# Kernel tuning notes

Measured on AMD Instinct MI355X. Metric: run time of the kernel, lower is better.

The kernel has to match this reference:

```python
import itertools, math
import jax, jax.numpy as jnp
import numpy as np

N_QUBITS = 8
N_LAYERS = 2
D = 2 ** N_QUBITS
B = 16384
PAIRS = list(itertools.combinations(range(N_QUBITS), 2))
N_PAIRS = len(PAIRS)


def _static():
    s = np.arange(D)
    # ising_masks[p, s] = +1 if bits qi,qj of s differ else -1
    masks = np.stack([
        np.where((((s >> (N_QUBITS - 1 - qi)) & 1) ^ ((s >> (N_QUBITS - 1 - qj)) & 1)).astype(bool), 1.0, -1.0).astype(np.float32)
        for qi, qj in PAIRS])
    # z_signs[k, s] = +1 if bit k of s is 0 else -1
    zsig = np.stack([
        np.where(((s >> (N_QUBITS - 1 - k)) & 1).astype(bool), -1.0, 1.0).astype(np.float32)
        for k in range(N_QUBITS)])
    # CNOT is a permutation: src[i] = i ^ target_mask if ctrl bit of i set, else i
    cidx = np.empty((N_LAYERS, N_QUBITS, D), np.int32)
    for l in range(N_LAYERS):
        rng = l % (N_QUBITS - 1) + 1 if N_QUBITS > 1 else 1
        for ctrl in range(N_QUBITS):
            tgt = (ctrl + rng) % N_QUBITS
            bit = ((s >> (N_QUBITS - 1 - ctrl)) & 1).astype(bool)
            cidx[l, ctrl] = np.where(bit, s ^ (1 << (N_QUBITS - 1 - tgt)), s)
    return jnp.asarray(masks), jnp.asarray(zsig), jnp.asarray(cidx)

ISING_MASKS, Z_SIGNS, CNOT_IDX = _static()


def _ry(a):
    # a: [...] -> [..., 2, 2] complex64
    c, sn = jnp.cos(a * 0.5), jnp.sin(a * 0.5)
    return jnp.stack([jnp.stack([c, -sn], -1), jnp.stack([sn, c], -1)], -2).astype(jnp.complex64)


def _rz(a):
    h = a.astype(jnp.complex64) * 0.5
    z = jnp.zeros_like(h)
    return jnp.stack([jnp.stack([jnp.exp(-1j * h), z], -1), jnp.stack([z, jnp.exp(1j * h)], -1)], -2)


def _rot(w):
    # w: [3] = (phi, theta, omega) -> Rot = RZ(omega) @ RY(theta) @ RZ(phi), shape [2,2]
    return _rz(w[2]) @ _ry(w[1]) @ _rz(w[0])


def _apply_1q(state, gate, k):
    # state: [B, D]; gate: [B,2,2] (batched) or [2,2] (shared)
    Bs, Ds = state.shape
    hi, lo = 1 << k, 1 << (N_QUBITS - k - 1)
    s = state.reshape(Bs, hi, 2, lo)
    if gate.ndim == 3:
        s = jnp.einsum('bij,bhjl->bhil', gate, s)
    else:
        s = jnp.einsum('ij,bhjl->bhil', gate, s)
    return s.reshape(Bs, Ds)


def _forward(theta, phi_enc, j_upper, vqc_weights):
    Bs = theta.shape[0]
    state = jnp.zeros((Bs, D), jnp.complex64).at[:, 0].set(1.0)
    # encoding layer
    for k in range(N_QUBITS):
        state = _apply_1q(state, _ry(theta[:, k]), k)
        state = _apply_1q(state, _rz(phi_enc[:, k]), k)
    # IsingZZ: product over pairs of exp(0.5j*pi*J_p*mask_p) == exp of sum
    exponent = (0.5 * math.pi) * (j_upper @ ISING_MASKS)  # [B, D], real
    state = state * jnp.exp(1j * exponent.astype(jnp.complex64))
    for l in range(N_LAYERS):
        for k in range(N_QUBITS):
            state = _apply_1q(state, _rot(vqc_weights[l, k]), k)
        for k in range(N_QUBITS):
            # CNOT ring as gather permutation (same math as state @ cnot.mT)
            state = jnp.take(state, CNOT_IDX[l, k], axis=1)
        if l < N_LAYERS - 1:
            for k in range(N_QUBITS):
                state = _apply_1q(state, _ry(theta[:, k] * 0.5), k)
                state = _apply_1q(state, _rz(phi_enc[:, k] * 0.5), k)
    probs = jnp.abs(state) ** 2  # [B, D] float32
    return (probs @ Z_SIGNS.T).astype(theta.dtype)  # [B, N_QUBITS]


def setup_inputs() -> dict:
    key = jax.random.key(0)
    k1, k2, k3, k4 = jax.random.split(key, 4)
    return {
        'theta': jax.random.normal(k1, (B, N_QUBITS), jnp.float32),
        'phi_enc': jax.random.normal(k2, (B, N_QUBITS), jnp.float32),
        'j_upper': jax.random.normal(k3, (B, N_PAIRS), jnp.float32),
        'vqc_weights': jax.random.normal(k4, (N_LAYERS, N_QUBITS, 3), jnp.float32),
    }


def reference(theta, phi_enc, j_upper, vqc_weights):
    return _forward(theta, phi_enc, j_upper, vqc_weights)
```

## Files before the change

### kernel.cpp

```cpp
#include <hip/hip_runtime.h>


using f2 = __attribute__((ext_vector_type(2))) float;

__device__ __forceinline__ f2 pkfma(f2 a, f2 b, f2 c) {
#if __has_builtin(__builtin_elementwise_fma)
    return __builtin_elementwise_fma(a, b, c);
#else
    f2 r; r.x = fmaf(a.x, b.x, c.x); r.y = fmaf(a.y, b.y, c.y); return r;
#endif
}

__device__ __forceinline__ f2 cmul2(f2 w, f2 z) {
    const f2 wr = (f2){w.x, w.x};
    const f2 wi = (f2){-w.y, w.y};
    const f2 zs = (f2){z.y, z.x};
    return pkfma(wi, zs, wr * z);
}
__device__ __forceinline__ f2 cmadd(f2 acc, f2 w, f2 z) {
    const f2 wr = (f2){w.x, w.x};
    const f2 wi = (f2){-w.y, w.y};
    const f2 zs = (f2){z.y, z.x};
    return pkfma(wi, zs, pkfma(wr, z, acc));
}

__device__ __forceinline__ f2 shflx(f2 v, int m) {
    f2 r; r.x = __shfl_xor(v.x, m, 64); r.y = __shfl_xor(v.y, m, 64); return r;
}

__device__ __forceinline__ f2 enc_sel(float t, float p, bool hi) {
    float s_, c_, sp_, cp_;
    __sincosf(t * 0.5f, &s_, &c_);
    __sincosf(p * 0.5f, &sp_, &cp_);
    const float m = hi ? s_ : c_;
    f2 r; r.x = m * cp_; r.y = hi ? m * sp_ : -m * sp_;
    return r;
}

template<int VREG, int VLANE, int UREG, int ULANE>
__device__ __forceinline__ void gate16(f2 (&s)[16], int lane16,
                                       f2 g00, f2 g01, f2 g10, f2 g11)
{
    f2 a0, b0, a1, b1;
    if constexpr (ULANE != 0) {
        const bool lp = (__popc(lane16 & ULANE) & 1) != 0;
        a0 = lp ? g11 : g00;  b0 = lp ? g10 : g01;
        a1 = lp ? g00 : g11;  b1 = lp ? g01 : g10;
    } else {
        a0 = g00; b0 = g01; a1 = g11; b1 = g10;
    }
    constexpr bool flip = (__builtin_popcount(VREG & UREG) & 1) != 0;
    if constexpr (VLANE == 0) {
        constexpr int pivot = VREG & (-VREG);
        #pragma unroll
        for (int j = 0; j < 16; ++j) {
            if ((j & pivot) != 0) continue;
            const int j2 = j ^ VREG;
            const bool cJ = (__builtin_popcount(j & UREG) & 1) != 0;
            const bool cK = cJ ^ flip;
            const f2 x = s[j], y = s[j2];
            const f2 A = cJ ? a1 : a0, B = cJ ? b1 : b0;
            const f2 C = cK ? a1 : a0, D = cK ? b1 : b0;
            s[j]  = cmadd(cmul2(A, x), B, y);
            s[j2] = cmadd(cmul2(C, y), D, x);
        }
    } else if constexpr (VREG == 0) {
        #pragma unroll
        for (int j = 0; j < 16; ++j) {
            const f2 p = shflx(s[j], VLANE);
            const bool cJ = (__builtin_popcount(j & UREG) & 1) != 0;
            const f2 A = cJ ? a1 : a0, B = cJ ? b1 : b0;
            s[j] = cmadd(cmul2(A, s[j]), B, p);
        }
    } else {
        constexpr int pivot = VREG & (-VREG);
        #pragma unroll
        for (int j = 0; j < 16; ++j) {
            if ((j & pivot) != 0) continue;
            const int j2 = j ^ VREG;
            const f2 p1 = shflx(s[j2], VLANE);
            const f2 p2 = shflx(s[j],  VLANE);
            const bool cJ = (__builtin_popcount(j & UREG) & 1) != 0;
            const bool cK = cJ ^ flip;
            const f2 A = cJ ? a1 : a0, B = cJ ? b1 : b0;
            const f2 C = cK ? a1 : a0, D = cK ? b1 : b0;
            s[j]  = cmadd(cmul2(A, s[j]),  B, p1);
            s[j2] = cmadd(cmul2(C, s[j2]), D, p2);
        }
    }
}

#define ROT0(K, VR, VL, UR, UL) do {                                    \
    const float* g_ = gates + (K)*8;                                    \
    const f2 R00={g_[0],g_[1]}, R01={g_[2],g_[3]};                      \
    const f2 R10={g_[4],g_[5]}, R11={g_[6],g_[7]};                      \
    gate16<VR, VL, UR, UL>(s, lane16, R00, R01, R10, R11);              \
} while (0)

#define FUSED(K, VR, VL, UR, UL) do {                                   \
    const float* g_ = gates + (8 + (K))*8;                              \
    const f2 R00={g_[0],g_[1]}, R01={g_[2],g_[3]};                      \
    const f2 R10={g_[4],g_[5]}, R11={g_[6],g_[7]};                      \
    float c_, s_, cp_, sp_;                                             \
    __sincosf(th[K] * 0.25f, &s_, &c_);                                 \
    __sincosf(ph[K] * 0.25f, &sp_, &cp_);                               \
    const f2 E00={ c_*cp_, -c_*sp_}, E01={-s_*cp_,  s_*sp_};            \
    const f2 E10={ s_*cp_,  s_*sp_}, E11={ c_*cp_,  c_*sp_};            \
    const f2 F00 = cmadd(cmul2(R00, E00), R01, E10);                    \
    const f2 F01 = cmadd(cmul2(R00, E01), R01, E11);                    \
    const f2 F10 = cmadd(cmul2(R10, E00), R11, E10);                    \
    const f2 F11 = cmadd(cmul2(R10, E01), R11, E11);                    \
    gate16<VR, VL, UR, UL>(s, lane16, F00, F01, F10, F11);              \
} while (0)

__global__ __launch_bounds__(64) void prep_gates(const float* __restrict__ w,
                                                 float* __restrict__ g)
{
    const int t = threadIdx.x;
    if (t < 16) {
        const float wph = w[t*3+0], wth = w[t*3+1], wom = w[t*3+2];
        float c_, s_, ca_, sa_, cb_, sb_;
        __sincosf(wth * 0.5f, &s_, &c_);
        __sincosf(0.5f * (wph + wom), &sa_, &ca_);
        __sincosf(0.5f * (wph - wom), &sb_, &cb_);
        float* o = g + t * 8;
        o[0] =  c_*ca_;  o[1] = -c_*sa_;
        o[2] = -s_*cb_;  o[3] = -s_*sb_;
        o[4] =  s_*cb_;  o[5] = -s_*sb_;
        o[6] =  c_*ca_;  o[7] =  c_*sa_;
    }
}

__global__ __launch_bounds__(64, 4) void vqc_kernel(
    const float* __restrict__ theta,
    const float* __restrict__ phi,
    const float* __restrict__ jup,
    const float* __restrict__ gates,
    float* __restrict__ out,
    int Btot)
{
    const int wid    = blockIdx.x;
    const int lane   = threadIdx.x & 63;
    const int lane16 = lane & 15;
    const int bq     = wid * 4 + (lane >> 4);
    const int b      = bq < Btot ? bq : Btot - 1;

    float th[8], ph[8];
    {
        const float4* t4 = reinterpret_cast<const float4*>(theta + (size_t)b * 8);
        const float4* p4 = reinterpret_cast<const float4*>(phi   + (size_t)b * 8);
        const float4 a = t4[0], c = t4[1], d = p4[0], e = p4[1];
        th[0]=a.x; th[1]=a.y; th[2]=a.z; th[3]=a.w;
        th[4]=c.x; th[5]=c.y; th[6]=c.z; th[7]=c.w;
        ph[0]=d.x; ph[1]=d.y; ph[2]=d.z; ph[3]=d.w;
        ph[4]=e.x; ph[5]=e.y; ph[6]=e.z; ph[7]=e.w;
    }

    f2 P = enc_sel(th[4], ph[4], (lane16 & 8) != 0);
    P = cmul2(P, enc_sel(th[5], ph[5], (lane16 & 4) != 0));
    P = cmul2(P, enc_sel(th[6], ph[6], (lane16 & 2) != 0));
    P = cmul2(P, enc_sel(th[7], ph[7], (lane16 & 1) != 0));

    f2 m01[4], m23[4];
    {
        float s0, c0, sp0, cp0, s1, c1, sp1, cp1;
        __sincosf(th[0]*0.5f, &s0, &c0); __sincosf(ph[0]*0.5f, &sp0, &cp0);
        __sincosf(th[1]*0.5f, &s1, &c1); __sincosf(ph[1]*0.5f, &sp1, &cp1);
        const f2 A0={c0*cp0,-c0*sp0}, A1={s0*cp0,s0*sp0};
        const f2 B0={c1*cp1,-c1*sp1}, B1={s1*cp1,s1*sp1};
        #pragma unroll
        for (int a = 0; a < 4; ++a)
            m01[a] = cmul2((a & 2) ? A1 : A0, (a & 1) ? B1 : B0);
        __sincosf(th[2]*0.5f, &s0, &c0); __sincosf(ph[2]*0.5f, &sp0, &cp0);
        __sincosf(th[3]*0.5f, &s1, &c1); __sincosf(ph[3]*0.5f, &sp1, &cp1);
        const f2 C0={c0*cp0,-c0*sp0}, C1={s0*cp0,s0*sp0};
        const f2 D0={c1*cp1,-c1*sp1}, D1={s1*cp1,s1*sp1};
        #pragma unroll
        for (int a = 0; a < 4; ++a)
            m23[a] = cmul2((a & 2) ? C1 : C0, (a & 1) ? D1 : D0);
    }

    float c01, c02, c03, c12, c13, c23, Q0, Q1, Q2, Q3, LL;
    {
        const float4* J4 = reinterpret_cast<const float4*>(jup + (size_t)b * 28);
        const float z4 = (lane16 & 8) ? -1.f : 1.f;
        const float z5 = (lane16 & 4) ? -1.f : 1.f;
        const float z6 = (lane16 & 2) ? -1.f : 1.f;
        const float z7 = (lane16 & 1) ? -1.f : 1.f;
        const float4 x0 = J4[0], x1 = J4[1], x2 = J4[2], x3 = J4[3];
        const float4 x4 = J4[4], x5 = J4[5], x6 = J4[6];
        c01 = x0.x; c02 = x0.y; c03 = x0.z;
        Q0  = x0.w*z4 + x1.x*z5 + x1.y*z6 + x1.z*z7;
        c12 = x1.w; c13 = x2.x;
        Q1  = x2.y*z4 + x2.z*z5 + x2.w*z6 + x3.x*z7;
        c23 = x3.y;
        Q2  = x3.z*z4 + x3.w*z5 + x4.x*z6 + x4.y*z7;
        Q3  = x4.z*z4 + x4.w*z5 + x5.x*z6 + x5.y*z7;
        LL  = x5.z*(z4*z5) + x5.w*(z4*z6) + x6.x*(z4*z7)
            + x6.y*(z5*z6) + x6.z*(z5*z7) + x6.w*(z6*z7);
    }

    f2 s[16];
    constexpr float HPI = 1.5707963267948966f;
    #pragma unroll
    for (int j = 0; j < 16; ++j) {
        f2 u = cmul2(cmul2(m01[j >> 2], m23[j & 3]), P);
        float S = LL;
        S += ((__builtin_popcount(j & 0xC) & 1) ? -c01 : c01);
        S += ((__builtin_popcount(j & 0xA) & 1) ? -c02 : c02);
        S += ((__builtin_popcount(j & 0x9) & 1) ? -c03 : c03);
        S += ((__builtin_popcount(j & 0x6) & 1) ? -c12 : c12);
        S += ((__builtin_popcount(j & 0x5) & 1) ? -c13 : c13);
        S += ((__builtin_popcount(j & 0x3) & 1) ? -c23 : c23);
        S += ((j & 8) ? -Q0 : Q0);
        S += ((j & 4) ? -Q1 : Q1);
        S += ((j & 2) ? -Q2 : Q2);
        S += ((j & 1) ? -Q3 : Q3);
        float se, ce;
        __sincosf(-HPI * S, &se, &ce);
        s[j] = cmul2(u, (f2){ce, se});
    }

    ROT0(0, 0x8, 0x0, 0x8, 0x0);
    ROT0(1, 0x4, 0x0, 0x4, 0x0);
    ROT0(2, 0x2, 0x0, 0x2, 0x0);
    ROT0(3, 0x1, 0x0, 0x1, 0x0);
    ROT0(4, 0x0, 0x8, 0x0, 0x8);
    ROT0(5, 0x0, 0x4, 0x0, 0x4);
    ROT0(6, 0x0, 0x2, 0x0, 0x2);
    ROT0(7, 0x0, 0x1, 0x0, 0x1);

    FUSED(0, 0xC, 0x0, 0x7, 0xF);
    FUSED(1, 0x6, 0x0, 0xC, 0x0);
    FUSED(2, 0x3, 0x0, 0xE, 0x0);
    FUSED(3, 0x1, 0x8, 0xF, 0x0);
    FUSED(4, 0x0, 0xC, 0xF, 0x8);
    FUSED(5, 0x0, 0x6, 0xF, 0xC);
    FUSED(6, 0x0, 0x3, 0xF, 0xE);
    FUSED(7, 0xC, 0x1, 0xF, 0xF);

    float p[16];
    #pragma unroll
    for (int j = 0; j < 16; ++j) p[j] = s[j].x*s[j].x + s[j].y*s[j].y;
    #pragma unroll
    for (int st = 1; st < 16; st <<= 1) {
        #pragma unroll
        for (int j = 0; j < 16; ++j) {
            if ((j & st) != 0) continue;
            const float a = p[j], bb = p[j | st];
            p[j] = a + bb;  p[j | st] = a - bb;
        }
    }
    float o[8];
    o[0] = (__popc(lane16 & 0x6) & 1) ? -p[0xE] : p[0xE];
    o[1] = (__popc(lane16 & 0x3) & 1) ? -p[0xF] : p[0xF];
    o[2] = (__popc(lane16 & 0xF) & 1) ? -p[0x9] : p[0x9];
    o[3] = p[0x3];
    o[4] = (__popc(lane16 & 0x7) & 1) ? -p[0x6] : p[0x6];
    o[5] = (__popc(lane16 & 0xC) & 1) ? -p[0xC] : p[0xC];
    o[6] = (__popc(lane16 & 0x9) & 1) ? -p[0x9] : p[0x9];
    o[7] = (__popc(lane16 & 0x3) & 1) ? -p[0x3] : p[0x3];

    #pragma unroll
    for (int m = 1; m <= 8; m <<= 1) {
        #pragma unroll
        for (int q = 0; q < 8; ++q) o[q] += __shfl_xor(o[q], m, 64);
    }

    if (lane16 == 0 && bq < Btot) {
        float4* op = reinterpret_cast<float4*>(out + (size_t)bq * 8);
        op[0] = make_float4(o[0], o[1], o[2], o[3]);
        op[1] = make_float4(o[4], o[5], o[6], o[7]);
    }
}

extern "C" void kernel_launch(void* const* d_in, const int* in_sizes, int n_in,
                              void* d_out, int out_size, void* d_ws, size_t ws_size,
                              hipStream_t stream) {
    const float* theta = (const float*)d_in[0];
    const float* phi   = (const float*)d_in[1];
    const float* jup   = (const float*)d_in[2];
    const float* w     = (const float*)d_in[3];
    float* out   = (float*)d_out;
    float* gates = (float*)d_ws;

    const int B = in_sizes[0] / 8;
    hipLaunchKernelGGL(prep_gates, dim3(1), dim3(64), 0, stream, w, gates);

    const int blocks = (B + 3) / 4;
    hipLaunchKernelGGL(vqc_kernel, dim3(blocks), dim3(64), 0, stream,
                       theta, phi, jup, gates, out, B);
}
```

Measured before the change: 82.47 us.

## Store state as split real/imag packed pairs for packed FMA gate updates

The per-lane state changes from 16 interleaved complex values to 8 real and 8 imaginary float2 vectors, each packing two adjacent amplitudes. Gate application is rewritten so each update is a chain of packed FMAs, with no swizzles or sign-flip vectors per complex multiply. Gates acting on the lowest register bit now swap the two halves within a vector. The aim is fewer VALU instructions per gate on packed-math hardware, at the cost of more template cases and extra shuffles for the swapped halves.

```diff
diff --git a/kernel.cpp b/kernel.cpp
--- a/kernel.cpp
+++ b/kernel.cpp
@@ -4,24 +4,19 @@
 using f2 = __attribute__((ext_vector_type(2))) float;
 
 __device__ __forceinline__ f2 pkfma(f2 a, f2 b, f2 c) {
-#if __has_builtin(__builtin_elementwise_fma)
     return __builtin_elementwise_fma(a, b, c);
-#else
-    f2 r; r.x = fmaf(a.x, b.x, c.x); r.y = fmaf(a.y, b.y, c.y); return r;
-#endif
 }
 
 __device__ __forceinline__ f2 cmul2(f2 w, f2 z) {
-    const f2 wr = (f2){w.x, w.x};
-    const f2 wi = (f2){-w.y, w.y};
-    const f2 zs = (f2){z.y, z.x};
-    return pkfma(wi, zs, wr * z);
+    f2 r;
+    r.x = w.x * z.x - w.y * z.y;
+    r.y = w.x * z.y + w.y * z.x;
+    return r;
 }
 __device__ __forceinline__ f2 cmadd(f2 acc, f2 w, f2 z) {
-    const f2 wr = (f2){w.x, w.x};
-    const f2 wi = (f2){-w.y, w.y};
-    const f2 zs = (f2){z.y, z.x};
-    return pkfma(wi, zs, pkfma(wr, z, acc));
+    acc.x += w.x * z.x - w.y * z.y;
+    acc.y += w.x * z.y + w.y * z.x;
+    return acc;
 }
 
 __device__ __forceinline__ f2 shflx(f2 v, int m) {
@@ -37,9 +32,21 @@
     return r;
 }
 
+#define UPD(c, xR, xI, yR, yI, oR, oI) do {                \
+    f2 t_ = Ar[c] * (xR);                                  \
+    t_ = pkfma(-Ai[c], (xI), t_);                          \
+    t_ = pkfma( Br[c], (yR), t_);                          \
+    const f2 nR_ = pkfma(-Bi[c], (yI), t_);                \
+    f2 u_ = Ar[c] * (xI);                                  \
+    u_ = pkfma( Ai[c], (xR), u_);                          \
+    u_ = pkfma( Br[c], (yI), u_);                          \
+    (oI) = pkfma( Bi[c], (yR), u_);                        \
+    (oR) = nR_;                                            \
+} while (0)
+
 template<int VREG, int VLANE, int UREG, int ULANE>
-__device__ __forceinline__ void gate16(f2 (&s)[16], int lane16,
-                                       f2 g00, f2 g01, f2 g10, f2 g11)
+__device__ __forceinline__ void gateS(f2 (&R)[8], f2 (&I)[8], int lane16,
+                                      f2 g00, f2 g01, f2 g10, f2 g11)
 {
     f2 a0, b0, a1, b1;
     if constexpr (ULANE != 0) {
@@ -49,43 +56,84 @@
     } else {
         a0 = g00; b0 = g01; a1 = g11; b1 = g10;
     }
-    constexpr bool flip = (__builtin_popcount(VREG & UREG) & 1) != 0;
-    if constexpr (VLANE == 0) {
-        constexpr int pivot = VREG & (-VREG);
-        #pragma unroll
-        for (int j = 0; j < 16; ++j) {
-            if ((j & pivot) != 0) continue;
-            const int j2 = j ^ VREG;
-            const bool cJ = (__builtin_popcount(j & UREG) & 1) != 0;
-            const bool cK = cJ ^ flip;
-            const f2 x = s[j], y = s[j2];
-            const f2 A = cJ ? a1 : a0, B = cJ ? b1 : b0;
-            const f2 C = cK ? a1 : a0, D = cK ? b1 : b0;
-            s[j]  = cmadd(cmul2(A, x), B, y);
-            s[j2] = cmadd(cmul2(C, y), D, x);
-        }
-    } else if constexpr (VREG == 0) {
-        #pragma unroll
-        for (int j = 0; j < 16; ++j) {
-            const f2 p = shflx(s[j], VLANE);
-            const bool cJ = (__builtin_popcount(j & UREG) & 1) != 0;
-            const f2 A = cJ ? a1 : a0, B = cJ ? b1 : b0;
-            s[j] = cmadd(cmul2(A, s[j]), B, p);
-        }
+    constexpr bool mix = (UREG & 1) != 0;
+    f2 Ar[2], Ai[2], Br[2], Bi[2];
+    if constexpr (mix) {
+        Ar[0]=(f2){a0.x,a1.x}; Ai[0]=(f2){a0.y,a1.y};
+        Br[0]=(f2){b0.x,b1.x}; Bi[0]=(f2){b0.y,b1.y};
+        Ar[1]=(f2){a1.x,a0.x}; Ai[1]=(f2){a1.y,a0.y};
+        Br[1]=(f2){b1.x,b0.x}; Bi[1]=(f2){b1.y,b0.y};
     } else {
-        constexpr int pivot = VREG & (-VREG);
-        #pragma unroll
-        for (int j = 0; j < 16; ++j) {
-            if ((j & pivot) != 0) continue;
-            const int j2 = j ^ VREG;
-            const f2 p1 = shflx(s[j2], VLANE);
-            const f2 p2 = shflx(s[j],  VLANE);
-            const bool cJ = (__builtin_popcount(j & UREG) & 1) != 0;
-            const bool cK = cJ ^ flip;
-            const f2 A = cJ ? a1 : a0, B = cJ ? b1 : b0;
-            const f2 C = cK ? a1 : a0, D = cK ? b1 : b0;
-            s[j]  = cmadd(cmul2(A, s[j]),  B, p1);
-            s[j2] = cmadd(cmul2(C, s[j2]), D, p2);
+        Ar[0]=(f2){a0.x,a0.x}; Ai[0]=(f2){a0.y,a0.y};
+        Br[0]=(f2){b0.x,b0.x}; Bi[0]=(f2){b0.y,b0.y};
+        Ar[1]=(f2){a1.x,a1.x}; Ai[1]=(f2){a1.y,a1.y};
+        Br[1]=(f2){b1.x,b1.x}; Bi[1]=(f2){b1.y,b1.y};
+    }
+    constexpr int PM  = VREG >> 1;
+    constexpr int UH  = UREG >> 1;
+    constexpr bool SW = (VREG & 1) != 0;
+
+    if constexpr (VREG == 0) {
+        #pragma unroll
+        for (int m = 0; m < 8; ++m) {
+            const int c = __builtin_popcount(m & UH) & 1;
+            const f2 pR = shflx(R[m], VLANE), pI = shflx(I[m], VLANE);
+            UPD(c, R[m], I[m], pR, pI, R[m], I[m]);
+        }
+    } else if constexpr (VLANE == 0 && !SW) {
+        constexpr int pivot = PM & (-PM);
+        #pragma unroll
+        for (int m = 0; m < 8; ++m) {
+            if (m & pivot) continue;
+            const int m2 = m ^ PM;
+            const int c  = __builtin_popcount(m  & UH) & 1;
+            const int c2 = __builtin_popcount(m2 & UH) & 1;
+            const f2 xR=R[m], xI=I[m], yR=R[m2], yI=I[m2];
+            UPD(c,  xR, xI, yR, yI, R[m],  I[m]);
+            UPD(c2, yR, yI, xR, xI, R[m2], I[m2]);
+        }
+    } else if constexpr (VLANE == 0 && SW && PM == 0) {
+        #pragma unroll
+        for (int m = 0; m < 8; ++m) {
+            const int c = __builtin_popcount(m & UH) & 1;
+            const f2 xR=R[m], xI=I[m];
+            const f2 yR=(f2){xR.y,xR.x}, yI=(f2){xI.y,xI.x};
+            UPD(c, xR, xI, yR, yI, R[m], I[m]);
+        }
+    } else if constexpr (VLANE == 0 && SW) {
+        constexpr int pivot = PM & (-PM);
+        #pragma unroll
+        for (int m = 0; m < 8; ++m) {
+            if (m & pivot) continue;
+            const int m2 = m ^ PM;
+            const int c  = __builtin_popcount(m  & UH) & 1;
+            const int c2 = __builtin_popcount(m2 & UH) & 1;
+            const f2 xR=R[m], xI=I[m], yR=R[m2], yI=I[m2];
+            const f2 ysR=(f2){yR.y,yR.x}, ysI=(f2){yI.y,yI.x};
+            const f2 xsR=(f2){xR.y,xR.x}, xsI=(f2){xI.y,xI.x};
+            UPD(c,  xR, xI, ysR, ysI, R[m],  I[m]);
+            UPD(c2, yR, yI, xsR, xsI, R[m2], I[m2]);
+        }
+    } else if constexpr (SW) {
+        #pragma unroll
+        for (int m = 0; m < 8; ++m) {
+            const int c = __builtin_popcount(m & UH) & 1;
+            const f2 pR = shflx(R[m], VLANE), pI = shflx(I[m], VLANE);
+            const f2 sR=(f2){pR.y,pR.x}, sI=(f2){pI.y,pI.x};
+            UPD(c, R[m], I[m], sR, sI, R[m], I[m]);
+        }
+    } else {
+        constexpr int pivot = PM & (-PM);
+        #pragma unroll
+        for (int m = 0; m < 8; ++m) {
+            if (m & pivot) continue;
+            const int m2 = m ^ PM;
+            const int c  = __builtin_popcount(m  & UH) & 1;
+            const int c2 = __builtin_popcount(m2 & UH) & 1;
+            const f2 p1R = shflx(R[m2], VLANE), p1I = shflx(I[m2], VLANE);
+            const f2 p2R = shflx(R[m],  VLANE), p2I = shflx(I[m],  VLANE);
+            UPD(c,  R[m],  I[m],  p1R, p1I, R[m],  I[m]);
+            UPD(c2, R[m2], I[m2], p2R, p2I, R[m2], I[m2]);
         }
     }
 }
@@ -94,7 +142,7 @@
     const float* g_ = gates + (K)*8;                                    \
     const f2 R00={g_[0],g_[1]}, R01={g_[2],g_[3]};                      \
     const f2 R10={g_[4],g_[5]}, R11={g_[6],g_[7]};                      \
-    gate16<VR, VL, UR, UL>(s, lane16, R00, R01, R10, R11);              \
+    gateS<VR, VL, UR, UL>(R, I, lane16, R00, R01, R10, R11);            \
 } while (0)
 
 #define FUSED(K, VR, VL, UR, UL) do {                                   \
@@ -110,7 +158,7 @@
     const f2 F01 = cmadd(cmul2(R00, E01), R01, E11);                    \
     const f2 F10 = cmadd(cmul2(R10, E00), R11, E10);                    \
     const f2 F11 = cmadd(cmul2(R10, E01), R11, E11);                    \
-    gate16<VR, VL, UR, UL>(s, lane16, F00, F01, F10, F11);              \
+    gateS<VR, VL, UR, UL>(R, I, lane16, F00, F01, F10, F11);            \
 } while (0)
 
 __global__ __launch_bounds__(64) void prep_gates(const float* __restrict__ w,
@@ -200,25 +248,32 @@
             + x6.y*(z5*z6) + x6.z*(z5*z7) + x6.w*(z6*z7);
     }
 
-    f2 s[16];
+    f2 R[8], I[8];
     constexpr float HPI = 1.5707963267948966f;
     #pragma unroll
-    for (int j = 0; j < 16; ++j) {
-        f2 u = cmul2(cmul2(m01[j >> 2], m23[j & 3]), P);
-        float S = LL;
-        S += ((__builtin_popcount(j & 0xC) & 1) ? -c01 : c01);
-        S += ((__builtin_popcount(j & 0xA) & 1) ? -c02 : c02);
-        S += ((__builtin_popcount(j & 0x9) & 1) ? -c03 : c03);
-        S += ((__builtin_popcount(j & 0x6) & 1) ? -c12 : c12);
-        S += ((__builtin_popcount(j & 0x5) & 1) ? -c13 : c13);
-        S += ((__builtin_popcount(j & 0x3) & 1) ? -c23 : c23);
-        S += ((j & 8) ? -Q0 : Q0);
-        S += ((j & 4) ? -Q1 : Q1);
-        S += ((j & 2) ? -Q2 : Q2);
-        S += ((j & 1) ? -Q3 : Q3);
-        float se, ce;
-        __sincosf(-HPI * S, &se, &ce);
-        s[j] = cmul2(u, (f2){ce, se});
+    for (int m = 0; m < 8; ++m) {
+        f2 amp[2];
+        #pragma unroll
+        for (int h = 0; h < 2; ++h) {
+            const int j = 2 * m + h;
+            f2 u = cmul2(cmul2(m01[j >> 2], m23[j & 3]), P);
+            float S = LL;
+            S += ((__builtin_popcount(j & 0xC) & 1) ? -c01 : c01);
+            S += ((__builtin_popcount(j & 0xA) & 1) ? -c02 : c02);
+            S += ((__builtin_popcount(j & 0x9) & 1) ? -c03 : c03);
+            S += ((__builtin_popcount(j & 0x6) & 1) ? -c12 : c12);
+            S += ((__builtin_popcount(j & 0x5) & 1) ? -c13 : c13);
+            S += ((__builtin_popcount(j & 0x3) & 1) ? -c23 : c23);
+            S += ((j & 8) ? -Q0 : Q0);
+            S += ((j & 4) ? -Q1 : Q1);
+            S += ((j & 2) ? -Q2 : Q2);
+            S += ((j & 1) ? -Q3 : Q3);
+            float se, ce;
+            __sincosf(-HPI * S, &se, &ce);
+            amp[h] = cmul2(u, (f2){ce, se});
+        }
+        R[m] = (f2){amp[0].x, amp[1].x};
+        I[m] = (f2){amp[0].y, amp[1].y};
     }
 
     ROT0(0, 0x8, 0x0, 0x8, 0x0);
@@ -241,7 +296,11 @@
 
     float p[16];
     #pragma unroll
-    for (int j = 0; j < 16; ++j) p[j] = s[j].x*s[j].x + s[j].y*s[j].y;
+    for (int m = 0; m < 8; ++m) {
+        const f2 t = pkfma(I[m], I[m], R[m] * R[m]);
+        p[2*m]   = t.x;
+        p[2*m+1] = t.y;
+    }
     #pragma unroll
     for (int st = 1; st < 16; st <<= 1) {
         #pragma unroll
```

New measurement: 83.33 us. No clear change (+1.0%).

## Exploit SU(2) gate structure to apply gates with four scalars and sign flips

Applied to the files above, without the earlier changes.

Gates are now represented by four scalars (g00 real/imag, g01 real/imag) using the unitary structure g10 = -conj(g01), g11 = conj(g00). Per-lane selection between gate variants is replaced by XOR sign-bit masks, and the gate application uses scalar fmaf chains instead of packed-float helpers. The prep kernel writes half as much gate data, and a float4 load replaces eight scalar loads. This cuts selects and register pressure, at the cost of giving up packed FMA instructions.

```diff
diff --git a/kernel.cpp b/kernel.cpp
--- a/kernel.cpp
+++ b/kernel.cpp
@@ -3,29 +3,24 @@
 
 using f2 = __attribute__((ext_vector_type(2))) float;
 
-__device__ __forceinline__ f2 pkfma(f2 a, f2 b, f2 c) {
-#if __has_builtin(__builtin_elementwise_fma)
-    return __builtin_elementwise_fma(a, b, c);
-#else
-    f2 r; r.x = fmaf(a.x, b.x, c.x); r.y = fmaf(a.y, b.y, c.y); return r;
-#endif
-}
-
 __device__ __forceinline__ f2 cmul2(f2 w, f2 z) {
-    const f2 wr = (f2){w.x, w.x};
-    const f2 wi = (f2){-w.y, w.y};
-    const f2 zs = (f2){z.y, z.x};
-    return pkfma(wi, zs, wr * z);
+    f2 r;
+    r.x = w.x * z.x - w.y * z.y;
+    r.y = w.x * z.y + w.y * z.x;
+    return r;
 }
 __device__ __forceinline__ f2 cmadd(f2 acc, f2 w, f2 z) {
-    const f2 wr = (f2){w.x, w.x};
-    const f2 wi = (f2){-w.y, w.y};
-    const f2 zs = (f2){z.y, z.x};
-    return pkfma(wi, zs, pkfma(wr, z, acc));
+    acc.x += w.x * z.x - w.y * z.y;
+    acc.y += w.x * z.y + w.y * z.x;
+    return acc;
 }
 
 __device__ __forceinline__ f2 shflx(f2 v, int m) {
     f2 r; r.x = __shfl_xor(v.x, m, 64); r.y = __shfl_xor(v.y, m, 64); return r;
+}
+
+__device__ __forceinline__ float uxor(float f, unsigned u) {
+    return __uint_as_float(__float_as_uint(f) ^ u);
 }
 
 __device__ __forceinline__ f2 enc_sel(float t, float p, bool hi) {
@@ -37,40 +32,39 @@
     return r;
 }
 
-template<int VREG, int VLANE, int UREG, int ULANE>
-__device__ __forceinline__ void gate16(f2 (&s)[16], int lane16,
-                                       f2 g00, f2 g01, f2 g10, f2 g11)
+template<int VREG, int VLANE, int UREG>
+__device__ __forceinline__ void gateU(f2 (&s)[16],
+                                      float g00r, float giP, float brP, float g01i)
 {
-    f2 a0, b0, a1, b1;
-    if constexpr (ULANE != 0) {
-        const bool lp = (__popc(lane16 & ULANE) & 1) != 0;
-        a0 = lp ? g11 : g00;  b0 = lp ? g10 : g01;
-        a1 = lp ? g00 : g11;  b1 = lp ? g01 : g10;
-    } else {
-        a0 = g00; b0 = g01; a1 = g11; b1 = g10;
-    }
-    constexpr bool flip = (__builtin_popcount(VREG & UREG) & 1) != 0;
     if constexpr (VLANE == 0) {
         constexpr int pivot = VREG & (-VREG);
         #pragma unroll
         for (int j = 0; j < 16; ++j) {
             if ((j & pivot) != 0) continue;
             const int j2 = j ^ VREG;
-            const bool cJ = (__builtin_popcount(j & UREG) & 1) != 0;
-            const bool cK = cJ ^ flip;
             const f2 x = s[j], y = s[j2];
-            const f2 A = cJ ? a1 : a0, B = cJ ? b1 : b0;
-            const f2 C = cK ? a1 : a0, D = cK ? b1 : b0;
-            s[j]  = cmadd(cmul2(A, x), B, y);
-            s[j2] = cmadd(cmul2(C, y), D, x);
+            {
+                const bool n = (__builtin_popcount(j & UREG) & 1) != 0;
+                const float gi = n ? -giP : giP, br = n ? -brP : brP;
+                s[j].x = fmaf(-g01i, y.y, fmaf(br, y.x, fmaf(-gi, x.y, g00r * x.x)));
+                s[j].y = fmaf( g01i, y.x, fmaf(br, y.y, fmaf( gi, x.x, g00r * x.y)));
+            }
+            {
+                const bool n = (__builtin_popcount(j2 & UREG) & 1) != 0;
+                const float gi = n ? -giP : giP, br = n ? -brP : brP;
+                s[j2].x = fmaf(-g01i, x.y, fmaf(br, x.x, fmaf(-gi, y.y, g00r * y.x)));
+                s[j2].y = fmaf( g01i, x.x, fmaf(br, x.y, fmaf( gi, y.x, g00r * y.y)));
+            }
         }
     } else if constexpr (VREG == 0) {
         #pragma unroll
         for (int j = 0; j < 16; ++j) {
-            const f2 p = shflx(s[j], VLANE);
-            const bool cJ = (__builtin_popcount(j & UREG) & 1) != 0;
-            const f2 A = cJ ? a1 : a0, B = cJ ? b1 : b0;
-            s[j] = cmadd(cmul2(A, s[j]), B, p);
+            const f2 w = shflx(s[j], VLANE);
+            const f2 x = s[j];
+            const bool n = (__builtin_popcount(j & UREG) & 1) != 0;
+            const float gi = n ? -giP : giP, br = n ? -brP : brP;
+            s[j].x = fmaf(-g01i, w.y, fmaf(br, w.x, fmaf(-gi, x.y, g00r * x.x)));
+            s[j].y = fmaf( g01i, w.x, fmaf(br, w.y, fmaf( gi, x.x, g00r * x.y)));
         }
     } else {
         constexpr int pivot = VREG & (-VREG);
@@ -80,37 +74,39 @@
             const int j2 = j ^ VREG;
             const f2 p1 = shflx(s[j2], VLANE);
             const f2 p2 = shflx(s[j],  VLANE);
-            const bool cJ = (__builtin_popcount(j & UREG) & 1) != 0;
-            const bool cK = cJ ^ flip;
-            const f2 A = cJ ? a1 : a0, B = cJ ? b1 : b0;
-            const f2 C = cK ? a1 : a0, D = cK ? b1 : b0;
-            s[j]  = cmadd(cmul2(A, s[j]),  B, p1);
-            s[j2] = cmadd(cmul2(C, s[j2]), D, p2);
-        }
-    }
-}
-
-#define ROT0(K, VR, VL, UR, UL) do {                                    \
-    const float* g_ = gates + (K)*8;                                    \
-    const f2 R00={g_[0],g_[1]}, R01={g_[2],g_[3]};                      \
-    const f2 R10={g_[4],g_[5]}, R11={g_[6],g_[7]};                      \
-    gate16<VR, VL, UR, UL>(s, lane16, R00, R01, R10, R11);              \
+            const f2 x = s[j], y = s[j2];
+            {
+                const bool n = (__builtin_popcount(j & UREG) & 1) != 0;
+                const float gi = n ? -giP : giP, br = n ? -brP : brP;
+                s[j].x = fmaf(-g01i, p1.y, fmaf(br, p1.x, fmaf(-gi, x.y, g00r * x.x)));
+                s[j].y = fmaf( g01i, p1.x, fmaf(br, p1.y, fmaf( gi, x.x, g00r * x.y)));
+            }
+            {
+                const bool n = (__builtin_popcount(j2 & UREG) & 1) != 0;
+                const float gi = n ? -giP : giP, br = n ? -brP : brP;
+                s[j2].x = fmaf(-g01i, p2.y, fmaf(br, p2.x, fmaf(-gi, y.y, g00r * y.x)));
+                s[j2].y = fmaf( g01i, p2.x, fmaf(br, p2.y, fmaf( gi, y.x, g00r * y.y)));
+            }
+        }
+    }
+}
+
+#define ROT0(K, VR, VL, UR, SL) do {                                    \
+    const float4 g_ = *reinterpret_cast<const float4*>(gates + (K)*4);  \
+    gateU<VR, VL, UR>(s, g_.x, uxor(g_.y, SL), uxor(g_.z, SL), g_.w);   \
 } while (0)
 
-#define FUSED(K, VR, VL, UR, UL) do {                                   \
-    const float* g_ = gates + (8 + (K))*8;                              \
-    const f2 R00={g_[0],g_[1]}, R01={g_[2],g_[3]};                      \
-    const f2 R10={g_[4],g_[5]}, R11={g_[6],g_[7]};                      \
+#define FUSED(K, VR, VL, UR, SL) do {                                   \
+    const float4 g_ = *reinterpret_cast<const float4*>(gates + (8+(K))*4); \
+    const f2 R00 = {g_.x, g_.y}, R01 = {g_.z, g_.w};                    \
     float c_, s_, cp_, sp_;                                             \
     __sincosf(th[K] * 0.25f, &s_, &c_);                                 \
     __sincosf(ph[K] * 0.25f, &sp_, &cp_);                               \
-    const f2 E00={ c_*cp_, -c_*sp_}, E01={-s_*cp_,  s_*sp_};            \
-    const f2 E10={ s_*cp_,  s_*sp_}, E11={ c_*cp_,  c_*sp_};            \
+    const f2 E00 = { c_*cp_, -c_*sp_}, E10 = { s_*cp_,  s_*sp_};        \
+    const f2 E01 = {-s_*cp_,  s_*sp_}, E11 = { c_*cp_,  c_*sp_};        \
     const f2 F00 = cmadd(cmul2(R00, E00), R01, E10);                    \
     const f2 F01 = cmadd(cmul2(R00, E01), R01, E11);                    \
-    const f2 F10 = cmadd(cmul2(R10, E00), R11, E10);                    \
-    const f2 F11 = cmadd(cmul2(R10, E01), R11, E11);                    \
-    gate16<VR, VL, UR, UL>(s, lane16, F00, F01, F10, F11);              \
+    gateU<VR, VL, UR>(s, F00.x, uxor(F00.y, SL), uxor(F01.x, SL), F01.y); \
 } while (0)
 
 __global__ __launch_bounds__(64) void prep_gates(const float* __restrict__ w,
@@ -123,11 +119,9 @@
         __sincosf(wth * 0.5f, &s_, &c_);
         __sincosf(0.5f * (wph + wom), &sa_, &ca_);
         __sincosf(0.5f * (wph - wom), &sb_, &cb_);
-        float* o = g + t * 8;
+        float* o = g + t * 4;
         o[0] =  c_*ca_;  o[1] = -c_*sa_;
         o[2] = -s_*cb_;  o[3] = -s_*sb_;
-        o[4] =  s_*cb_;  o[5] = -s_*sb_;
-        o[6] =  c_*ca_;  o[7] =  c_*sa_;
     }
 }
 
@@ -156,6 +150,14 @@
         ph[4]=e.x; ph[5]=e.y; ph[6]=e.z; ph[7]=e.w;
     }
 
+    const unsigned s8 = (unsigned)(lane16 & 8) << 28;
+    const unsigned s4 = (unsigned)(lane16 & 4) << 29;
+    const unsigned s2 = (unsigned)(lane16 & 2) << 30;
+    const unsigned s1 = (unsigned)(lane16 & 1) << 31;
+    const unsigned sC = s8 ^ s4;
+    const unsigned sE = sC ^ s2;
+    const unsigned sF = sE ^ s1;
+
     f2 P = enc_sel(th[4], ph[4], (lane16 & 8) != 0);
     P = cmul2(P, enc_sel(th[5], ph[5], (lane16 & 4) != 0));
     P = cmul2(P, enc_sel(th[6], ph[6], (lane16 & 2) != 0));
@@ -163,18 +165,18 @@
 
     f2 m01[4], m23[4];
     {
-        float s0, c0, sp0, cp0, s1, c1, sp1, cp1;
+        float s0, c0, sp0, cp0, s1_, c1_, sp1, cp1;
         __sincosf(th[0]*0.5f, &s0, &c0); __sincosf(ph[0]*0.5f, &sp0, &cp0);
-        __sincosf(th[1]*0.5f, &s1, &c1); __sincosf(ph[1]*0.5f, &sp1, &cp1);
+        __sincosf(th[1]*0.5f, &s1_, &c1_); __sincosf(ph[1]*0.5f, &sp1, &cp1);
         const f2 A0={c0*cp0,-c0*sp0}, A1={s0*cp0,s0*sp0};
-        const f2 B0={c1*cp1,-c1*sp1}, B1={s1*cp1,s1*sp1};
+        const f2 B0={c1_*cp1,-c1_*sp1}, B1={s1_*cp1,s1_*sp1};
         #pragma unroll
         for (int a = 0; a < 4; ++a)
             m01[a] = cmul2((a & 2) ? A1 : A0, (a & 1) ? B1 : B0);
         __sincosf(th[2]*0.5f, &s0, &c0); __sincosf(ph[2]*0.5f, &sp0, &cp0);
-        __sincosf(th[3]*0.5f, &s1, &c1); __sincosf(ph[3]*0.5f, &sp1, &cp1);
+        __sincosf(th[3]*0.5f, &s1_, &c1_); __sincosf(ph[3]*0.5f, &sp1, &cp1);
         const f2 C0={c0*cp0,-c0*sp0}, C1={s0*cp0,s0*sp0};
-        const f2 D0={c1*cp1,-c1*sp1}, D1={s1*cp1,s1*sp1};
+        const f2 D0={c1_*cp1,-c1_*sp1}, D1={s1_*cp1,s1_*sp1};
         #pragma unroll
         for (int a = 0; a < 4; ++a)
             m23[a] = cmul2((a & 2) ? C1 : C0, (a & 1) ? D1 : D0);
@@ -221,27 +223,27 @@
         s[j] = cmul2(u, (f2){ce, se});
     }
 
-    ROT0(0, 0x8, 0x0, 0x8, 0x0);
-    ROT0(1, 0x4, 0x0, 0x4, 0x0);
-    ROT0(2, 0x2, 0x0, 0x2, 0x0);
-    ROT0(3, 0x1, 0x0, 0x1, 0x0);
-    ROT0(4, 0x0, 0x8, 0x0, 0x8);
-    ROT0(5, 0x0, 0x4, 0x0, 0x4);
-    ROT0(6, 0x0, 0x2, 0x0, 0x2);
-    ROT0(7, 0x0, 0x1, 0x0, 0x1);
-
-    FUSED(0, 0xC, 0x0, 0x7, 0xF);
-    FUSED(1, 0x6, 0x0, 0xC, 0x0);
-    FUSED(2, 0x3, 0x0, 0xE, 0x0);
-    FUSED(3, 0x1, 0x8, 0xF, 0x0);
-    FUSED(4, 0x0, 0xC, 0xF, 0x8);
-    FUSED(5, 0x0, 0x6, 0xF, 0xC);
-    FUSED(6, 0x0, 0x3, 0xF, 0xE);
-    FUSED(7, 0xC, 0x1, 0xF, 0xF);
+    ROT0(0, 0x8, 0x0, 0x8, 0u);
+    ROT0(1, 0x4, 0x0, 0x4, 0u);
+    ROT0(2, 0x2, 0x0, 0x2, 0u);
+    ROT0(3, 0x1, 0x0, 0x1, 0u);
+    ROT0(4, 0x0, 0x8, 0x0, s8);
+    ROT0(5, 0x0, 0x4, 0x0, s4);
+    ROT0(6, 0x0, 0x2, 0x0, s2);
+    ROT0(7, 0x0, 0x1, 0x0, s1);
+
+    FUSED(0, 0xC, 0x0, 0x7, sF);
+    FUSED(1, 0x6, 0x0, 0xC, 0u);
+    FUSED(2, 0x3, 0x0, 0xE, 0u);
+    FUSED(3, 0x1, 0x8, 0xF, 0u);
+    FUSED(4, 0x0, 0xC, 0xF, s8);
+    FUSED(5, 0x0, 0x6, 0xF, sC);
+    FUSED(6, 0x0, 0x3, 0xF, sE);
+    FUSED(7, 0xC, 0x1, 0xF, sF);
 
     float p[16];
     #pragma unroll
-    for (int j = 0; j < 16; ++j) p[j] = s[j].x*s[j].x + s[j].y*s[j].y;
+    for (int j = 0; j < 16; ++j) p[j] = fmaf(s[j].y, s[j].y, s[j].x * s[j].x);
     #pragma unroll
     for (int st = 1; st < 16; st <<= 1) {
         #pragma unroll
```

Result: no change. 81.90 us (-0.7%).
